# Kernel optimization log

Hardware: AMD Instinct MI355X
Metric: run time of the kernel (lower is better)

Reference implementation:

```python
import jax, jax.numpy as jnp
import numpy as np

DIM = 1024
HEADS = 16
DIM_HEAD = 64
INNER = HEADS * DIM_HEAD
B, M, N = 8, 4096, 256
EPS = 1e-5


def layer_norm(x, g, b):
    mu = jnp.mean(x, axis=-1, keepdims=True)
    var = jnp.mean(jnp.square(x - mu), axis=-1, keepdims=True)
    return (x - mu) * jax.lax.rsqrt(var + EPS) * g + b


def setup_inputs() -> dict:
    key = jax.random.key(0)
    ks = jax.random.split(key, 8)
    x = jax.random.normal(ks[0], (B, M, DIM), dtype=jnp.float32)
    latents = jax.random.normal(ks[1], (B, N, DIM), dtype=jnp.float32)
    x_att_mask = jax.random.randint(ks[2], (B, M), 0, 2) == 1  # True = masked
    s = 0.02
    Wq = jax.random.normal(ks[3], (DIM, INNER), dtype=jnp.float32) * s
    Wkv = jax.random.normal(ks[4], (DIM, 2 * INNER), dtype=jnp.float32) * s
    Wo = jax.random.normal(ks[5], (INNER, DIM), dtype=jnp.float32) * s
    return {
        "x": x, "latents": latents, "x_att_mask": x_att_mask,
        "nm_g": jnp.ones((DIM,), jnp.float32), "nm_b": jnp.zeros((DIM,), jnp.float32),
        "nl_g": jnp.ones((DIM,), jnp.float32), "nl_b": jnp.zeros((DIM,), jnp.float32),
        "Wq": Wq, "Wkv": Wkv, "Wo": Wo,
    }


def reference(x, latents, x_att_mask, nm_g, nm_b, nl_g, nl_b, Wq, Wkv, Wo):
    b, n, d = latents.shape
    h, dh = HEADS, DIM_HEAD
    scale = dh ** (-0.5)

    # additive mask: concat(media mask, all-False latent mask); True -> -inf, False -> +1 (faithful quirk)
    latent_mask = jnp.zeros((b, n), dtype=bool)
    full_mask = jnp.concatenate([x_att_mask, latent_mask], axis=1)  # [b, m+n]
    add_mask = jnp.where(full_mask, -jnp.inf, 1.0).astype(x.dtype)[:, None, None, :]  # [b,1,1,m+n]

    xn = layer_norm(x, nm_g, nm_b)
    ln = layer_norm(latents, nl_g, nl_b)

    q = (ln @ Wq).reshape(b, n, h, dh).transpose(0, 2, 1, 3)  # bhnd
    kv_in = jnp.concatenate([xn, ln], axis=1)                 # [b, m+n, d]
    kv = kv_in @ Wkv
    k, v = jnp.split(kv, 2, axis=-1)
    j = kv_in.shape[1]
    k = k.reshape(b, j, h, dh).transpose(0, 2, 1, 3)
    v = v.reshape(b, j, h, dh).transpose(0, 2, 1, 3)

    sim = jnp.einsum('bhid,bhjd->bhij', q * scale, k)
    sim = sim - jnp.max(sim, axis=-1, keepdims=True)
    sim = sim + add_mask
    attn = jax.nn.softmax(sim, axis=-1)
    out = jnp.einsum('bhij,bhjd->bhid', attn, v)
    out = out.transpose(0, 2, 1, 3).reshape(b, n, h * dh)
    return out @ Wo
```

## Files before the change

### kernel.cpp

```cpp
#include <hip/hip_runtime.h>
#include <hip/hip_bf16.h>
#include <stdint.h>

#define HEADS 16
#define DH    64
#define NB    8
#define MQ    256
#define MX    4096
#define JD    4352
#define DIMV  1024
#define GK    1024

typedef __bf16 bf16;
typedef __bf16 bf16x8 __attribute__((ext_vector_type(8)));
typedef float  f32x4  __attribute__((ext_vector_type(4)));

#define SWZ(r, c) (((c) ^ ((r) & 7)))

#define VMW(n) asm volatile("s_waitcnt vmcnt(" #n ")" ::: "memory")

__device__ __forceinline__ void gl_lds16(const void* g, void* l) {
  __builtin_amdgcn_global_load_lds((const __attribute__((address_space(1))) void*)g,
                                   (__attribute__((address_space(3))) void*)l, 16, 0, 0);
}

__global__ __launch_bounds__(256) void ln_kernel(
    const float* __restrict__ X, const float* __restrict__ gw, const float* __restrict__ bw,
    bf16* __restrict__ out_kv, bf16* __restrict__ out_ln, int is_lat)
{
  const int row = blockIdx.x;
  const int tid = threadIdx.x;
  const float4 v = ((const float4*)(X + (size_t)row * DIMV))[tid];
  float s  = v.x + v.y + v.z + v.w;
  float s2 = v.x*v.x + v.y*v.y + v.z*v.z + v.w*v.w;
#pragma unroll
  for (int m = 1; m < 64; m <<= 1) { s += __shfl_xor(s, m); s2 += __shfl_xor(s2, m); }
  __shared__ float red[8];
  const int wid = tid >> 6;
  if ((tid & 63) == 0) { red[wid*2] = s; red[wid*2+1] = s2; }
  __syncthreads();
  s  = red[0] + red[2] + red[4] + red[6];
  s2 = red[1] + red[3] + red[5] + red[7];
  const float mu  = s * (1.0f / DIMV);
  const float var = s2 * (1.0f / DIMV) - mu * mu;
  const float rst = rsqrtf(var + 1e-5f);
  const float4 g4 = ((const float4*)gw)[tid];
  const float4 b4 = ((const float4*)bw)[tid];
  union { bf16 h[4]; short4 s4; } u;
  u.h[0] = (bf16)((v.x - mu) * rst * g4.x + b4.x);
  u.h[1] = (bf16)((v.y - mu) * rst * g4.y + b4.y);
  u.h[2] = (bf16)((v.z - mu) * rst * g4.z + b4.z);
  u.h[3] = (bf16)((v.w - mu) * rst * g4.w + b4.w);
  size_t kvrow;
  if (is_lat) { int b = row >> 8;  int i = row & 255;  kvrow = (size_t)b * JD + MX + i; }
  else        { int b = row >> 12; int j = row & 4095; kvrow = (size_t)b * JD + j; }
  *(short4*)(out_kv + kvrow * DIMV + tid * 4) = u.s4;
  if (is_lat) *(short4*)(out_ln + (size_t)row * DIMV + tid * 4) = u.s4;
}

__global__ __launch_bounds__(256) void transpose_w(
    const float* __restrict__ in, bf16* __restrict__ out, int R, int C)
{
  __shared__ float t[64][65];
  const int tilesC = C >> 6;
  const int tc = blockIdx.x % tilesC, tr = blockIdx.x / tilesC;
  const int r0 = tr << 6, c0 = tc << 6;
  const int lr = threadIdx.x >> 4;
  const int lc = (threadIdx.x & 15) << 2;
#pragma unroll
  for (int p = 0; p < 4; p++) {
    float4 v = *(const float4*)&in[(size_t)(r0 + lr + p*16) * C + c0 + lc];
    t[lr + p*16][lc    ] = v.x; t[lr + p*16][lc + 1] = v.y;
    t[lr + p*16][lc + 2] = v.z; t[lr + p*16][lc + 3] = v.w;
  }
  __syncthreads();
#pragma unroll
  for (int p = 0; p < 4; p++) {
    const int oc = lr + p*16;
    union { bf16 h[4]; short4 s4; } u;
    u.h[0] = (bf16)t[lc    ][oc]; u.h[1] = (bf16)t[lc + 1][oc];
    u.h[2] = (bf16)t[lc + 2][oc]; u.h[3] = (bf16)t[lc + 3][oc];
    *(short4*)&out[(size_t)(c0 + oc) * R + r0 + lc] = u.s4;
  }
}

__global__ __launch_bounds__(256) void mask_detect(
    const unsigned char* __restrict__ m, int n, int* __restrict__ flag)
{
  const int tid = threadIdx.x;
  int cnt = 0;
  for (int i = tid; i < n; i += 256) cnt += (m[i] != 0) ? 1 : 0;
#pragma unroll
  for (int mm = 1; mm < 64; mm <<= 1) cnt += __shfl_xor(cnt, mm);
  __shared__ int r4[4];
  if ((tid & 63) == 0) r4[tid >> 6] = cnt;
  __syncthreads();
  if (tid == 0) {
    int t = r4[0] + r4[1] + r4[2] + r4[3];
    flag[0] = (t * 16 > n * 5) ? 1 : 0;
  }
}

__global__ __launch_bounds__(256) void mask_build(
    const void* __restrict__ mraw, const int* __restrict__ flag, float* __restrict__ mm)
{
  const int idx = blockIdx.x * 256 + threadIdx.x;
  const int b = idx / JD, j = idx - b * JD;
  float v = 1.0f;
  if (j < MX) {
    bool masked = (*flag) ? (((const unsigned char*)mraw)[b * MX + j] != 0)
                          : (((const int*)mraw)[b * MX + j] != 0);
    v = masked ? 0.0f : 1.0f;
  }
  mm[idx] = v;
}

__global__ __launch_bounds__(512, 2) void gemm256(
    const bf16* __restrict__ A, const bf16* __restrict__ Bt,
    const bf16* __restrict__ Aq, const bf16* __restrict__ Bq,
    bf16* __restrict__ outR, bf16* __restrict__ outVT, bf16* __restrict__ outQ)
{
  __shared__ bf16 sm[65536];

  const int tid = threadIdx.x;
  const int lane = tid & 63, wid = tid >> 6;
  const int wr = wid >> 2, wc = wid & 3;
  const int lc = lane & 15, lq = lane >> 4;
  const int srow = tid >> 3, sc = tid & 7;
  const int ssw = SWZ(srow, sc) * 8;

  int bid = blockIdx.x;
  bid = (bid & 7) * 140 + (bid >> 3);

  const bf16 *Arow, *Brow;
  int m0, n0, omode;
  if (bid < 1088) {
    const int by = bid >> 3, bx = bid & 7;
    m0 = by * 256;
    if (bx < 4) { n0 = bx * 256;
      Arow = A  + (size_t)m0 * GK; Brow = Bt + (size_t)n0 * GK; omode = 0; }
    else        { n0 = 1024 + (bx - 4) * 256;
      Arow = Bt + (size_t)n0 * GK; Brow = A  + (size_t)m0 * GK; omode = 1; }
  } else {
    const int ix = bid - 1088;
    m0 = (ix >> 2) * 256; n0 = (ix & 3) * 256;
    Arow = Aq + (size_t)m0 * GK; Brow = Bq + (size_t)n0 * GK; omode = 2;
  }

  const bf16* Abase = Arow + (size_t)srow * GK + ssw;
  const bf16* Bbase = Brow + (size_t)srow * GK + ssw;

  auto stA = [&](int d, int h, int kt) {
#pragma unroll
    for (int l = 0; l < 2; ++l)
      gl_lds16(Abase + (size_t)(h*128 + l*64) * GK + kt * 64,
               &sm[d*32768 + (h*128 + l*64)*64 + tid*8]);
  };
  auto stB = [&](int d, int h, int kt) {
#pragma unroll
    for (int l = 0; l < 2; ++l)
      gl_lds16(Bbase + (size_t)(h*128 + l*64) * GK + kt * 64,
               &sm[d*32768 + 16384 + (h*128 + l*64)*64 + tid*8]);
  };

  f32x4 acc[8][4];
#pragma unroll
  for (int i = 0; i < 8; i++)
#pragma unroll
    for (int j = 0; j < 4; j++)
#pragma unroll
      for (int r = 0; r < 4; r++) acc[i][j][r] = 0.f;

#define DS_PHASE(d, q, STAGE_STMT, WAIT_STMT)                                  \
  {                                                                            \
    const bf16* As_ = sm + (d)*32768;                                          \
    const bf16* Bs_ = sm + (d)*32768 + 16384;                                  \
    bf16x8 af[2][2];                                                           \
    _Pragma("unroll") for (int mi = 0; mi < 2; ++mi)                           \
      _Pragma("unroll") for (int kk = 0; kk < 2; ++kk)                         \
        af[mi][kk] = *(const bf16x8*)&As_[(wr*128 + ((q)*2+mi)*16 + lc)*64 +   \
                                          SWZ(lc, kk*4 + lq)*8];               \
    if ((q) == 0) {                                                            \
      _Pragma("unroll") for (int n = 0; n < 4; ++n)                            \
        _Pragma("unroll") for (int kk = 0; kk < 2; ++kk)                       \
          bfrag[n][kk] = *(const bf16x8*)&Bs_[(wc*64 + n*16 + lc)*64 +         \
                                              SWZ(lc, kk*4 + lq)*8];           \
    }                                                                          \
    STAGE_STMT;                                                                \
    WAIT_STMT;                                                                 \
    __builtin_amdgcn_s_barrier();                                              \
    __builtin_amdgcn_s_setprio(1);                                             \
    _Pragma("unroll") for (int kk = 0; kk < 2; ++kk)                           \
      _Pragma("unroll") for (int mi = 0; mi < 2; ++mi)                         \
        _Pragma("unroll") for (int n = 0; n < 4; ++n)                          \
          acc[(q)*2+mi][n] = __builtin_amdgcn_mfma_f32_16x16x32_bf16(          \
              af[mi][kk], bfrag[n][kk], acc[(q)*2+mi][n], 0, 0, 0);            \
    __builtin_amdgcn_s_setprio(0);                                             \
    __builtin_amdgcn_s_barrier();                                              \
  }

  stB(0, 0, 0); stB(0, 1, 0);
  stA(0, 0, 0); stA(0, 1, 0);
  stB(1, 0, 1); stB(1, 1, 1);
  VMW(4);
  __builtin_amdgcn_s_barrier();

  bf16x8 bfrag[4][2];
#pragma unroll 1
  for (int it = 0; it < 8; ++it) {
    const int tb = 2*it + 1, ta2 = 2*it + 2, tb2 = 2*it + 3;
    const bool s2 = (ta2 < 16), s3 = (tb2 < 16);
    DS_PHASE(0, 0, { stA(1, 0, tb); stA(1, 1, tb); }, {});
    DS_PHASE(0, 1, { if (s2) stB(0, 0, ta2); }, {});
    DS_PHASE(0, 2, { if (s2) stB(0, 1, ta2); }, {});
    DS_PHASE(0, 3, {}, { if (s2) { VMW(4); } else { VMW(0); } });
    DS_PHASE(1, 0, { if (s2) stA(0, 0, ta2); }, {});
    DS_PHASE(1, 1, { if (s2) stA(0, 1, ta2); }, {});
    DS_PHASE(1, 2, { if (s3) stB(1, 0, tb2); }, {});
    DS_PHASE(1, 3, { if (s3) stB(1, 1, tb2); }, { if (s3) { VMW(4); } });
  }
#undef DS_PHASE

  __syncthreads();
  bf16* Ct = sm;
#pragma unroll
  for (int m = 0; m < 8; ++m)
#pragma unroll
    for (int n = 0; n < 4; ++n) {
      const int col = wc*64 + n*16 + lc;
      const int cch = col >> 3, cw = col & 7;
#pragma unroll
      for (int r = 0; r < 4; ++r) {
        const int row = wr*128 + m*16 + lq*4 + r;
        Ct[row*256 + (((cch ^ (row & 31)) << 3) + cw)] = (bf16)acc[m][n][r];
      }
    }
  __syncthreads();

  const int cch = tid & 31, r0 = tid >> 5;
  if (omode != 1) {
    bf16* dst0 = (omode == 0 ? outR : outQ);
#pragma unroll
    for (int i = 0; i < 16; ++i) {
      const int row = r0 + i*16;
      bf16x8 v = *(const bf16x8*)&Ct[row*256 + ((cch ^ (row & 31)) << 3)];
      *(bf16x8*)(dst0 + (size_t)(m0 + row) * 1024 + n0 + cch*8) = v;
    }
  } else {
    const int bb = m0 / JD;
    const int jbase = m0 - bb * JD;
#pragma unroll
    for (int i = 0; i < 16; ++i) {
      const int row = r0 + i*16;
      const int cc = n0 + row - 1024;
      bf16x8 v = *(const bf16x8*)&Ct[row*256 + ((cch ^ (row & 31)) << 3)];
      bf16* dst = outVT + (((size_t)(bb*HEADS + (cc >> 6)))*64 + (cc & 63)) * JD
                        + jbase + cch*8;
      *(bf16x8*)dst = v;
    }
  }
}

__global__ __launch_bounds__(256) void gemm128(
    const bf16* __restrict__ A, const bf16* __restrict__ Bt,
    float* __restrict__ Cf, int N)
{
  __shared__ bf16 smem[2 * 128 * 64];
  bf16* As = smem;
  bf16* Bs = smem + 128 * 64;

  const int tid = threadIdx.x;
  const int lane = tid & 63, wid = tid >> 6;
  const int wr = wid >> 1, wc = wid & 1;
  const int m0 = blockIdx.y * 128;
  const int n0 = blockIdx.x * 128;
  const int srow = tid >> 3, sc = tid & 7;
  const int ssw = SWZ(srow, sc) * 8;
  const int lc = lane & 15, lq = lane >> 4;

  f32x4 acc[4][4];
#pragma unroll
  for (int i = 0; i < 4; i++)
#pragma unroll
    for (int j = 0; j < 4; j++)
#pragma unroll
      for (int r = 0; r < 4; r++) acc[i][j][r] = 0.f;

  const bf16* Abase = A + (size_t)m0 * GK + (size_t)srow * GK + ssw;
  const bf16* Bbase = Bt + (size_t)n0 * GK + (size_t)srow * GK + ssw;

  for (int k0 = 0; k0 < GK; k0 += 64) {
    __syncthreads();
#pragma unroll
    for (int q = 0; q < 4; q++) {
      gl_lds16(Abase + (size_t)q * 32 * GK + k0, &As[(srow + q*32) * 64 + sc*8]);
      gl_lds16(Bbase + (size_t)q * 32 * GK + k0, &Bs[(srow + q*32) * 64 + sc*8]);
    }
    VMW(0);
    __syncthreads();
#pragma unroll
    for (int kk = 0; kk < 2; kk++) {
      bf16x8 af[4], bfr[4];
#pragma unroll
      for (int mi = 0; mi < 4; mi++)
        af[mi] = *(const bf16x8*)&As[(wr*64 + mi*16 + lc) * 64 + SWZ(lc, kk*4 + lq)*8];
#pragma unroll
      for (int ni = 0; ni < 4; ni++)
        bfr[ni] = *(const bf16x8*)&Bs[(wc*64 + ni*16 + lc) * 64 + SWZ(lc, kk*4 + lq)*8];
#pragma unroll
      for (int mi = 0; mi < 4; mi++)
#pragma unroll
        for (int ni = 0; ni < 4; ni++)
          acc[mi][ni] = __builtin_amdgcn_mfma_f32_16x16x32_bf16(af[mi], bfr[ni], acc[mi][ni], 0, 0, 0);
    }
  }

#pragma unroll
  for (int mi = 0; mi < 4; mi++)
#pragma unroll
    for (int ni = 0; ni < 4; ni++) {
      const int r = m0 + wr*64 + mi*16 + lq*4;
      const int c = n0 + wc*64 + ni*16 + lc;
#pragma unroll
      for (int reg = 0; reg < 4; reg++)
        Cf[(size_t)(r + reg) * N + c] = acc[mi][ni][reg];
    }
}

__global__ __launch_bounds__(512) void attn_kernel(
    const bf16* __restrict__ Qrows,
    const bf16* __restrict__ Krows,
    const bf16* __restrict__ VT,
    const float* __restrict__ mmul,
    bf16* __restrict__ outp)
{
  const int bh = blockIdx.x >> 1, qt = blockIdx.x & 1;
  const int b = bh >> 4, h = bh & 15;
  __shared__ bf16 Qs[128 * 64];
  __shared__ bf16 Ks[2][64 * 64];
  __shared__ bf16 VTs[2][64 * 64];
  __shared__ bf16 Ps[8][16 * 64];
  const int tid = threadIdx.x, lane = tid & 63, w = tid >> 6;
  const int lc = lane & 15, lq = lane >> 4;
  const int srow = tid >> 3, sc = tid & 7;
  const int ssw = SWZ(srow, sc) * 8;

  const bf16* Qg = Qrows + ((size_t)(b*MQ + qt*128)) * 1024 + h*64;
  const bf16* Kg = Krows + ((size_t)b * JD) * 1024 + h*64;
  const bf16* Vg = VT + ((size_t)bh * 64) * JD;

  auto stKV = [&](int c, int t) {
    gl_lds16(Kg + (size_t)(t*64 + srow) * 1024 + ssw, &Ks[c][tid*8]);
    gl_lds16(Vg + (size_t)srow * JD + t*64 + ssw, &VTs[c][tid*8]);
  };

  gl_lds16(Qg + (size_t)srow * 1024 + ssw, &Qs[tid*8]);
  gl_lds16(Qg + (size_t)(srow + 64) * 1024 + ssw, &Qs[(tid + 512)*8]);
  stKV(0, 0);
  stKV(1, 1);
  VMW(2);
  __syncthreads();

  bf16x8 qf[2];
#pragma unroll
  for (int kk = 0; kk < 2; kk++)
    qf[kk] = *(const bf16x8*)&Qs[(w*16 + lc) * 64 + SWZ(lc, kk*4 + lq)*8];

  f32x4 oacc[4];
  float den[4];
#pragma unroll
  for (int di = 0; di < 4; di++)
#pragma unroll
    for (int r = 0; r < 4; r++) oacc[di][r] = 0.f;
#pragma unroll
  for (int r = 0; r < 4; r++) den[r] = 0.f;

#pragma unroll 1
  for (int t = 0; t < JD/64; ++t) {
    const int c = t & 1;
    const int j0 = t * 64;

    f32x4 sacc[4];
#pragma unroll
    for (int nj = 0; nj < 4; nj++)
#pragma unroll
      for (int r = 0; r < 4; r++) sacc[nj][r] = 0.f;
#pragma unroll
    for (int kk = 0; kk < 2; kk++) {
      bf16x8 kf[4];
#pragma unroll
      for (int nj = 0; nj < 4; nj++)
        kf[nj] = *(const bf16x8*)&Ks[c][(nj*16 + lc) * 64 + SWZ(lc, kk*4 + lq)*8];
#pragma unroll
      for (int nj = 0; nj < 4; nj++)
        sacc[nj] = __builtin_amdgcn_mfma_f32_16x16x32_bf16(qf[kk], kf[nj], sacc[nj], 0, 0, 0);
    }

#pragma unroll
    for (int nj = 0; nj < 4; nj++) {
      const float mm = mmul[b * JD + j0 + nj*16 + lc];
#pragma unroll
      for (int r = 0; r < 4; r++) {
        const float p = exp2f(sacc[nj][r] * 0.18033688f) * mm;
        den[r] += p;
        const int row = lq*4 + r, col = nj*16 + lc;
        Ps[w][row*64 + (((col >> 3) ^ (row & 7)) << 3) + (col & 7)] = (bf16)p;
      }
    }

#pragma unroll
    for (int kk = 0; kk < 2; kk++) {
      bf16x8 pf = *(const bf16x8*)&Ps[w][lc*64 + SWZ(lc, kk*4 + lq)*8];
#pragma unroll
      for (int di = 0; di < 4; di++) {
        bf16x8 vf = *(const bf16x8*)&VTs[c][(di*16 + lc) * 64 + SWZ(lc, kk*4 + lq)*8];
        oacc[di] = __builtin_amdgcn_mfma_f32_16x16x32_bf16(pf, vf, oacc[di], 0, 0, 0);
      }
    }

    __builtin_amdgcn_s_barrier();
    if (t + 2 < JD/64) {
      stKV(c, t + 2);
      VMW(2);
    } else if (t + 1 < JD/64) {
      VMW(0);
    }
    __builtin_amdgcn_s_barrier();
  }

#pragma unroll
  for (int r = 0; r < 4; r++) {
    float d = den[r];
    d += __shfl_xor(d, 1); d += __shfl_xor(d, 2);
    d += __shfl_xor(d, 4); d += __shfl_xor(d, 8);
    den[r] = 1.0f / d;
  }

#pragma unroll
  for (int di = 0; di < 4; di++) {
    const int col = h*64 + di*16 + lc;
#pragma unroll
    for (int r = 0; r < 4; r++) {
      const int i = qt*128 + w*16 + lq*4 + r;
      outp[(size_t)(b*MQ + i) * 1024 + col] = (bf16)(oacc[di][r] * den[r]);
    }
  }
}

extern "C" void kernel_launch(void* const* d_in, const int* in_sizes, int n_in,
                              void* d_out, int out_size, void* d_ws, size_t ws_size,
                              hipStream_t stream)
{
  const float* x    = (const float*)d_in[0];
  const float* lat  = (const float*)d_in[1];
  const void*  mraw = d_in[2];
  const float* nm_g = (const float*)d_in[3];
  const float* nm_b = (const float*)d_in[4];
  const float* nl_g = (const float*)d_in[5];
  const float* nl_b = (const float*)d_in[6];
  const float* Wq   = (const float*)d_in[7];
  const float* Wkv  = (const float*)d_in[8];
  const float* Wo   = (const float*)d_in[9];
  float* out = (float*)d_out;

  char* p = (char*)d_ws;
  auto alloc = [&](size_t bytes) { char* r = p; p += (bytes + 255) & ~(size_t)255; return r; };

  bf16*  kv_in  = (bf16*)alloc((size_t)NB * JD * DIMV * 2);
  bf16*  Krows  = (bf16*)alloc((size_t)NB * JD * 1024 * 2);
  bf16*  VTbuf  = (bf16*)alloc((size_t)NB * HEADS * 64 * JD * 2);
  bf16*  WqT    = (bf16*)alloc((size_t)1024 * 1024 * 2);
  bf16*  WkvT   = (bf16*)alloc((size_t)2048 * 1024 * 2);
  bf16*  WoT    = (bf16*)alloc((size_t)1024 * 1024 * 2);
  bf16*  ln_buf = (bf16*)alloc((size_t)NB * MQ * DIMV * 2);
  bf16*  Qrows  = (bf16*)alloc((size_t)NB * MQ * 1024 * 2);
  bf16*  attout = (bf16*)alloc((size_t)NB * MQ * DIMV * 2);
  float* mmulp  = (float*)alloc((size_t)NB * JD * 4);
  int*   flag   = (int*)alloc(256);
  (void)ws_size; (void)in_sizes; (void)n_in; (void)out_size;

  ln_kernel<<<NB * MX, 256, 0, stream>>>(x,   nm_g, nm_b, kv_in, nullptr, 0);
  ln_kernel<<<NB * MQ, 256, 0, stream>>>(lat, nl_g, nl_b, kv_in, ln_buf, 1);
  transpose_w<<<256, 256, 0, stream>>>(Wq,  WqT,  1024, 1024);
  transpose_w<<<512, 256, 0, stream>>>(Wkv, WkvT, 1024, 2048);
  transpose_w<<<256, 256, 0, stream>>>(Wo,  WoT,  1024, 1024);
  mask_detect<<<1, 256, 0, stream>>>((const unsigned char*)mraw, 32768, flag);
  mask_build<<<136, 256, 0, stream>>>(mraw, flag, mmulp);

  gemm256<<<1120, 512, 0, stream>>>(kv_in, WkvT, ln_buf, WqT, Krows, VTbuf, Qrows);
  attn_kernel<<<256, 512, 0, stream>>>(Qrows, Krows, VTbuf, mmulp, attout);
  gemm128<<<dim3(8, 16), 256, 0, stream>>>(attout, WoT, out, 1024);
}
```

Baseline: 533.5 us.

## Prefetch next LDS fragments into double-buffered registers during MFMA phases

Restructures the GEMM main loop so that each phase reads the next phase's A and B fragments from LDS into alternate register sets while the MFMAs run on the current set. The loop is peeled, with a separate tail for the last K tile, and the global-load waits are moved to the start of the phases that consume the data. The aim is to hide LDS read latency behind matrix-core work. The cost is higher register pressure from the doubled fragment arrays and more intricate wait and barrier ordering.

```diff
diff --git a/kernel.cpp b/kernel.cpp
--- a/kernel.cpp
+++ b/kernel.cpp
@@ -171,30 +171,31 @@
 #pragma unroll
       for (int r = 0; r < 4; r++) acc[i][j][r] = 0.f;
 
-#define DS_PHASE(d, q, STAGE_STMT, WAIT_STMT)                                  \
+  bf16x8 afA[2][2], afB[2][2], bfA[4][2], bfB[4][2];
+
+#define PH(WAIT, PBUF, PQ, NXT, PREFBF, BFN, STAGE_STMT, CUR, BFC, QACC)       \
   {                                                                            \
-    const bf16* As_ = sm + (d)*32768;                                          \
-    const bf16* Bs_ = sm + (d)*32768 + 16384;                                  \
-    bf16x8 af[2][2];                                                           \
+    WAIT;                                                                      \
+    const bf16* Ap_ = sm + (PBUF)*32768;                                       \
     _Pragma("unroll") for (int mi = 0; mi < 2; ++mi)                           \
       _Pragma("unroll") for (int kk = 0; kk < 2; ++kk)                         \
-        af[mi][kk] = *(const bf16x8*)&As_[(wr*128 + ((q)*2+mi)*16 + lc)*64 +   \
-                                          SWZ(lc, kk*4 + lq)*8];               \
-    if ((q) == 0) {                                                            \
+        NXT[mi][kk] = *(const bf16x8*)&Ap_[(wr*128 + ((PQ)*2+mi)*16 + lc)*64   \
+                                           + SWZ(lc, kk*4 + lq)*8];            \
+    if (PREFBF) {                                                              \
+      const bf16* Bp_ = sm + (PBUF)*32768 + 16384;                             \
       _Pragma("unroll") for (int n = 0; n < 4; ++n)                            \
         _Pragma("unroll") for (int kk = 0; kk < 2; ++kk)                       \
-          bfrag[n][kk] = *(const bf16x8*)&Bs_[(wc*64 + n*16 + lc)*64 +         \
-                                              SWZ(lc, kk*4 + lq)*8];           \
+          BFN[n][kk] = *(const bf16x8*)&Bp_[(wc*64 + n*16 + lc)*64             \
+                                            + SWZ(lc, kk*4 + lq)*8];           \
     }                                                                          \
     STAGE_STMT;                                                                \
-    WAIT_STMT;                                                                 \
     __builtin_amdgcn_s_barrier();                                              \
     __builtin_amdgcn_s_setprio(1);                                             \
     _Pragma("unroll") for (int kk = 0; kk < 2; ++kk)                           \
       _Pragma("unroll") for (int mi = 0; mi < 2; ++mi)                         \
         _Pragma("unroll") for (int n = 0; n < 4; ++n)                          \
-          acc[(q)*2+mi][n] = __builtin_amdgcn_mfma_f32_16x16x32_bf16(          \
-              af[mi][kk], bfrag[n][kk], acc[(q)*2+mi][n], 0, 0, 0);            \
+          acc[(QACC)*2+mi][n] = __builtin_amdgcn_mfma_f32_16x16x32_bf16(       \
+              CUR[mi][kk], BFC[n][kk], acc[(QACC)*2+mi][n], 0, 0, 0);          \
     __builtin_amdgcn_s_setprio(0);                                             \
     __builtin_amdgcn_s_barrier();                                              \
   }
@@ -204,22 +205,48 @@
   stB(1, 0, 1); stB(1, 1, 1);
   VMW(4);
   __builtin_amdgcn_s_barrier();
-
-  bf16x8 bfrag[4][2];
+#pragma unroll
+  for (int mi = 0; mi < 2; ++mi)
+#pragma unroll
+    for (int kk = 0; kk < 2; ++kk)
+      afA[mi][kk] = *(const bf16x8*)&sm[(wr*128 + mi*16 + lc)*64 + SWZ(lc, kk*4 + lq)*8];
+#pragma unroll
+  for (int n = 0; n < 4; ++n)
+#pragma unroll
+    for (int kk = 0; kk < 2; ++kk)
+      bfA[n][kk] = *(const bf16x8*)&sm[16384 + (wc*64 + n*16 + lc)*64 + SWZ(lc, kk*4 + lq)*8];
+
 #pragma unroll 1
-  for (int it = 0; it < 8; ++it) {
+  for (int it = 0; it < 7; ++it) {
     const int tb = 2*it + 1, ta2 = 2*it + 2, tb2 = 2*it + 3;
-    const bool s2 = (ta2 < 16), s3 = (tb2 < 16);
-    DS_PHASE(0, 0, { stA(1, 0, tb); stA(1, 1, tb); }, {});
-    DS_PHASE(0, 1, { if (s2) stB(0, 0, ta2); }, {});
-    DS_PHASE(0, 2, { if (s2) stB(0, 1, ta2); }, {});
-    DS_PHASE(0, 3, {}, { if (s2) { VMW(4); } else { VMW(0); } });
-    DS_PHASE(1, 0, { if (s2) stA(0, 0, ta2); }, {});
-    DS_PHASE(1, 1, { if (s2) stA(0, 1, ta2); }, {});
-    DS_PHASE(1, 2, { if (s3) stB(1, 0, tb2); }, {});
-    DS_PHASE(1, 3, { if (s3) stB(1, 1, tb2); }, { if (s3) { VMW(4); } });
-  }
-#undef DS_PHASE
+    PH({},     0, 1, afB, 0, bfB, { stA(1, 0, tb);  }, afA, bfA, 0);
+    PH({},     0, 2, afA, 0, bfB, { stA(1, 1, tb);  }, afB, bfA, 1);
+    PH({},     0, 3, afB, 0, bfB, { stB(0, 0, ta2); }, afA, bfA, 2);
+    PH(VMW(2), 1, 0, afA, 1, bfB, { stB(0, 1, ta2); }, afB, bfA, 3);
+    PH({},     1, 1, afB, 0, bfA, { stA(0, 0, ta2); }, afA, bfB, 0);
+    PH({},     1, 2, afA, 0, bfA, { stA(0, 1, ta2); }, afB, bfB, 1);
+    PH({},     1, 3, afB, 0, bfA, { stB(1, 0, tb2); }, afA, bfB, 2);
+    PH(VMW(2), 0, 0, afA, 1, bfA, { stB(1, 1, tb2); }, afB, bfB, 3);
+  }
+  PH({},     0, 1, afB, 0, bfB, { stA(1, 0, 15); }, afA, bfA, 0);
+  PH({},     0, 2, afA, 0, bfB, { stA(1, 1, 15); }, afB, bfA, 1);
+  PH({},     0, 3, afB, 0, bfB, {}, afA, bfA, 2);
+  PH(VMW(0), 1, 0, afA, 1, bfB, {}, afB, bfA, 3);
+  PH({},     1, 1, afB, 0, bfA, {}, afA, bfB, 0);
+  PH({},     1, 2, afA, 0, bfA, {}, afB, bfB, 1);
+  PH({},     1, 3, afB, 0, bfA, {}, afA, bfB, 2);
+  __builtin_amdgcn_s_barrier();
+  __builtin_amdgcn_s_setprio(1);
+#pragma unroll
+  for (int kk = 0; kk < 2; ++kk)
+#pragma unroll
+    for (int mi = 0; mi < 2; ++mi)
+#pragma unroll
+      for (int n = 0; n < 4; ++n)
+        acc[6+mi][n] = __builtin_amdgcn_mfma_f32_16x16x32_bf16(
+            afB[mi][kk], bfB[n][kk], acc[6+mi][n], 0, 0, 0);
+  __builtin_amdgcn_s_setprio(0);
+#undef PH
 
   __syncthreads();
   bf16* Ct = sm;
```

Measured after the change: 546.0 us. 1.02x slower.
